# Kernel tuning notes

Measured on AMD Instinct MI355X. Metric: run time of the kernel, lower is better.

Reference implementation:

```python
import math
import jax, jax.numpy as jnp
import numpy as np

L, H, E, D = 12, 12, 768, 64   # stack_size, mh_size, embedding_dim, dim_w_matrices
B, S = 4, 512
EPS = 1e-5


def positional_enc(seq_len, model_dim):
    # faithful: power_ind = 10000 XOR int(2*i/dim)
    i = np.arange(model_dim)
    p = np.bitwise_xor(10000, (2 * i) // model_dim).astype(np.float32)
    pos = np.arange(seq_len, dtype=np.float32)[:, None]
    ang = pos / p[None, :]
    pe = np.where(i % 2 == 0, np.sin(ang), np.cos(ang)).astype(np.float32)
    return jnp.asarray(pe)


def layer_norm(x, g, b):
    mu = jnp.mean(x, axis=-1, keepdims=True)
    var = jnp.mean(jnp.square(x - mu), axis=-1, keepdims=True)
    return (x - mu) * jax.lax.rsqrt(var + EPS) * g + b


def encoder(x, wq, wo, g1, b1, fw, fb, g2, b2):
    # x: [B,S,E]; wq: [H,E,D]; wo: [E,H*D]; fw: [E,E] (torch Linear layout)
    bs = x.shape[0] * x.shape[1]
    nb = x.reshape(bs, E)                              # flatten batch (faithful)
    q = jnp.einsum('ne,hed->hnd', nb, wq)              # q == k == v (bug kept)
    scores = jax.nn.softmax(jnp.einsum('hnd,hmd->hnm', q, q) / math.sqrt(D), axis=-1)
    z = jnp.einsum('hnm,hmd->hnd', scores, q)          # [H,BS,D]
    zc = z.reshape(H * D, bs)                          # per-head view(D,-1) + cat
    mh = (wo @ zc).reshape(x.shape)                    # [B,S,E]
    l1 = layer_norm(x + mh, g1, b1)
    ffn = l1 @ fw.T + fb
    return layer_norm(l1 + ffn, g2, b2)


def setup_inputs() -> dict:
    key = jax.random.key(0)
    ks = jax.random.split(key, 8)

    def xavier(k, shape, fan_in, fan_out):
        lim = math.sqrt(6.0 / (fan_in + fan_out))
        return jax.random.uniform(k, shape, jnp.float32, -lim, lim)

    return {
        'tokens': jax.random.normal(ks[0], (B, S, E), jnp.float32),
        'wq':    xavier(ks[1], (L, H, E, D), E, D),
        'wo':    xavier(ks[2], (L, E, H * D), E, H * D),
        'ln1_g': jnp.ones((L, E), jnp.float32),
        'ln1_b': jnp.zeros((L, E), jnp.float32),
        'ffn_w': xavier(ks[3], (L, E, E), E, E),
        'ffn_b': jnp.zeros((L, E), jnp.float32),
        'ln2_g': jnp.ones((L, E), jnp.float32),
        'ln2_b': jnp.zeros((L, E), jnp.float32),
    }


def reference(tokens, wq, wo, ln1_g, ln1_b, ffn_w, ffn_b, ln2_g, ln2_b):
    pe = positional_enc(tokens.shape[1], tokens.shape[2])
    # faithful: layer 0 applied once on pe+tokens, then ALL layers (0 again) in loop
    x = encoder(pe + tokens, wq[0], wo[0], ln1_g[0], ln1_b[0],
                ffn_w[0], ffn_b[0], ln2_g[0], ln2_b[0])
    for l in range(L):
        x = encoder(x, wq[l], wo[l], ln1_g[l], ln1_b[l],
                    ffn_w[l], ffn_b[l], ln2_g[l], ln2_b[l])
    return x
```

## Files before the change

kernel.cpp:

```cpp
#include <hip/hip_runtime.h>
#include <hip/hip_bf16.h>


#define BS_TOK 2048
#define EMB 768
#define NH 12
#define HD 64
#define WQN (12 * NH * EMB * HD)

typedef __attribute__((ext_vector_type(8))) short bf16x8;
typedef __attribute__((ext_vector_type(4))) short bf16x4;
typedef __attribute__((ext_vector_type(4))) float f32x4;

__device__ __forceinline__ short f2bf(float f) {
  union { __hip_bfloat16 h; short s; } u;
  u.h = __float2bfloat16(f);
  return u.s;
}

#define MFMA16(a, b, c) __builtin_amdgcn_mfma_f32_16x16x32_bf16(a, b, c, 0, 0, 0)
#define SW64(r, k) ((r) * 64 + ((((k) >> 3) ^ ((r) & 7)) << 3) + ((k) & 7))
#define BAR() asm volatile("s_waitcnt lgkmcnt(0)\n\ts_barrier" ::: "memory")

__global__ __launch_bounds__(256) void cvt_weights_kernel(const float* __restrict__ wo,
                                                          const float* __restrict__ fw,
                                                          short* __restrict__ wob,
                                                          short* __restrict__ fwb) {
  const float* src = blockIdx.y ? fw : wo;
  short* dst = blockIdx.y ? fwb : wob;
  int i = (blockIdx.x * 256 + threadIdx.x) * 8;
  float4 a = *(const float4*)(src + i);
  float4 b = *(const float4*)(src + i + 4);
  bf16x8 t;
  t[0] = f2bf(a.x); t[1] = f2bf(a.y); t[2] = f2bf(a.z); t[3] = f2bf(a.w);
  t[4] = f2bf(b.x); t[5] = f2bf(b.y); t[6] = f2bf(b.z); t[7] = f2bf(b.w);
  *(bf16x8*)(dst + i) = t;
}

__global__ __launch_bounds__(256) void wq_trans_kernel(const float* __restrict__ wq,
                                                       short* __restrict__ wqT) {
  __shared__ short T[64 * 64];
  const int et = blockIdx.x;
  const int lh = blockIdx.y;
  const int tid = threadIdx.x;
  const float* src = wq + ((size_t)lh * EMB + et * 64) * HD;
  {
    int r = tid >> 2, c16 = (tid & 3) << 4;
    const float* p = src + r * HD + c16;
    float4 x0 = *(const float4*)(p + 0);
    float4 x1 = *(const float4*)(p + 4);
    float4 x2 = *(const float4*)(p + 8);
    float4 x3 = *(const float4*)(p + 12);
    bf16x8 a, b;
    a[0] = f2bf(x0.x); a[1] = f2bf(x0.y); a[2] = f2bf(x0.z); a[3] = f2bf(x0.w);
    a[4] = f2bf(x1.x); a[5] = f2bf(x1.y); a[6] = f2bf(x1.z); a[7] = f2bf(x1.w);
    b[0] = f2bf(x2.x); b[1] = f2bf(x2.y); b[2] = f2bf(x2.z); b[3] = f2bf(x2.w);
    b[4] = f2bf(x3.x); b[5] = f2bf(x3.y); b[6] = f2bf(x3.z); b[7] = f2bf(x3.w);
    int g = c16 >> 3;
    *(bf16x8*)&T[r * 64 + ((g ^ (r & 7)) << 3)] = a;
    *(bf16x8*)&T[r * 64 + (((g + 1) ^ (r & 7)) << 3)] = b;
  }
  __syncthreads();
  {
    int d = tid >> 2, e16 = (tid & 3) << 4;
    bf16x8 t0, t1;
#pragma unroll
    for (int j = 0; j < 8; ++j) t0[j] = T[SW64(e16 + j, d)];
#pragma unroll
    for (int j = 0; j < 8; ++j) t1[j] = T[SW64(e16 + 8 + j, d)];
    short* q = wqT + ((size_t)lh * HD + d) * EMB + et * 64 + e16;
    *(bf16x8*)(q) = t0;
    *(bf16x8*)(q + 8) = t1;
  }
}

__global__ __launch_bounds__(256) void pe_add_kernel(const float* __restrict__ tok,
                                                     float* __restrict__ X,
                                                     short* __restrict__ Xb) {
  int idx = blockIdx.x * 256 + threadIdx.x;
  int e = idx % EMB;
  int t = idx / EMB;
  int s = t & 511;
  float p = (e < 384) ? 10000.0f : 10001.0f;
  float ang = (float)s / p;
  float pe = (e & 1) ? cosf(ang) : sinf(ang);
  float v = tok[idx] + pe;
  X[idx] = v;
  Xb[idx] = f2bf(v);
}

__device__ __forceinline__ void load64(const short* __restrict__ src, int ld,
                                       int row0, int k0, bf16x8* r, int tid) {
  int rr = tid >> 2, kb = (tid & 3) << 4;
  const short* p = src + (size_t)(row0 + rr) * ld + k0 + kb;
  r[0] = *(const bf16x8*)(p);
  r[1] = *(const bf16x8*)(p + 8);
}
__device__ __forceinline__ void write64(short* dst, const bf16x8* r, int tid) {
  int rr = tid >> 2, g = (tid & 3) << 1;
  *(bf16x8*)&dst[rr * 64 + (((g + 0) ^ (rr & 7)) << 3)] = r[0];
  *(bf16x8*)&dst[rr * 64 + (((g + 1) ^ (rr & 7)) << 3)] = r[1];
}

__device__ __forceinline__ void load128(const short* __restrict__ src, int ld,
                                        int row0, int k0, bf16x8* r, int tid) {
  int rr = tid >> 1, kb = (tid & 1) << 5;
  const short* p = src + (size_t)(row0 + rr) * ld + k0 + kb;
  r[0] = *(const bf16x8*)(p);
  r[1] = *(const bf16x8*)(p + 8);
  r[2] = *(const bf16x8*)(p + 16);
  r[3] = *(const bf16x8*)(p + 24);
}
__device__ __forceinline__ void write128(short* dst, const bf16x8* r, int tid) {
  int rr = tid >> 1, g = (tid & 1) << 2;
#pragma unroll
  for (int i = 0; i < 4; ++i)
    *(bf16x8*)&dst[rr * 64 + (((g + i) ^ (rr & 7)) << 3)] = r[i];
}

__device__ __forceinline__ void load_zc(const short* __restrict__ Zcb,
                                        int k0, int col0, bf16x8 cr[2], int tid) {
  int kk = tid >> 2, nb = (tid & 3) << 4;
  const short* p = Zcb + (size_t)(k0 + kk) * BS_TOK + col0 + nb;
  cr[0] = *(const bf16x8*)(p);
  cr[1] = *(const bf16x8*)(p + 8);
}
__device__ __forceinline__ void write_zc(short* dst, const bf16x8 cr[2], int tid) {
  int kk = tid >> 2, nb = (tid & 3) << 4;
#pragma unroll
  for (int j = 0; j < 8; ++j) dst[SW64(nb + j, kk)] = cr[0][j];
#pragma unroll
  for (int j = 0; j < 8; ++j) dst[SW64(nb + 8 + j, kk)] = cr[1][j];
}

#define GEMM_TILE_COMPUTE(As, Bs, acc)                                              \
  {                                                                                 \
    _Pragma("unroll") for (int s = 0; s < 2; ++s) {                                 \
      int ra = (w << 4) + l15;                                                      \
      bf16x8 af = *(const bf16x8*)&As[ra * 64 + ((((s << 2) + quad) ^ (ra & 7)) << 3)]; \
      _Pragma("unroll") for (int nt = 0; nt < 4; ++nt) {                            \
        int rb = (nt << 4) + l15;                                                   \
        bf16x8 bf = *(const bf16x8*)&Bs[rb * 64 + ((((s << 2) + quad) ^ (rb & 7)) << 3)]; \
        acc[nt] = MFMA16(af, bf, acc[nt]);                                          \
      }                                                                             \
    }                                                                               \
  }

#define GEMM_TILE_COMPUTE2(As, Bs, acc)                                             \
  {                                                                                 \
    _Pragma("unroll") for (int s = 0; s < 2; ++s) {                                 \
      bf16x8 af[2];                                                                 \
      _Pragma("unroll") for (int u = 0; u < 2; ++u) {                               \
        int ra = (w << 5) + (u << 4) + l15;                                         \
        af[u] = *(const bf16x8*)&As[ra * 64 + ((((s << 2) + quad) ^ (ra & 7)) << 3)]; \
      }                                                                             \
      _Pragma("unroll") for (int nt = 0; nt < 4; ++nt) {                            \
        int rb = (nt << 4) + l15;                                                   \
        bf16x8 bf = *(const bf16x8*)&Bs[rb * 64 + ((((s << 2) + quad) ^ (rb & 7)) << 3)]; \
        acc[0][nt] = MFMA16(af[0], bf, acc[0][nt]);                                 \
        acc[1][nt] = MFMA16(af[1], bf, acc[1][nt]);                                 \
      }                                                                             \
    }                                                                               \
  }

__global__ __launch_bounds__(256) void gemm_q_kernel(const short* __restrict__ Xb,
                                                     const short* __restrict__ WqT,
                                                     short* __restrict__ Qo,
                                                     short* __restrict__ Qt) {
  __shared__ short As[2][64 * 64];
  __shared__ short Bs[2][64 * 64];
  const int m0 = blockIdx.x * 64;
  const int h = blockIdx.y;
  const int tid = threadIdx.x;
  const int w = tid >> 6, lane = tid & 63, l15 = lane & 15, quad = lane >> 4;
  const short* wqh = WqT + (size_t)h * (HD * EMB);
  f32x4 acc[4] = {};
  bf16x8 ar[2], br[2];
  load64(Xb, EMB, m0, 0, ar, tid);
  load64(wqh, EMB, 0, 0, br, tid);
  write64(As[0], ar, tid);
  write64(Bs[0], br, tid);
  load64(Xb, EMB, m0, 64, ar, tid);
  load64(wqh, EMB, 0, 64, br, tid);
  BAR();
  for (int k0 = 0; k0 < EMB; k0 += 64) {
    const int cur = (k0 >> 6) & 1;
    const short* Ac = As[cur];
    const short* Bc = Bs[cur];
    GEMM_TILE_COMPUTE(Ac, Bc, acc);
    if (k0 + 64 < EMB) {
      write64((short*)As[cur ^ 1], ar, tid);
      write64((short*)Bs[cur ^ 1], br, tid);
      if (k0 + 128 < EMB) {
        load64(Xb, EMB, m0, k0 + 128, ar, tid);
        load64(wqh, EMB, 0, k0 + 128, br, tid);
      }
    }
    BAR();
  }
  short* T = (short*)As[0];
#pragma unroll
  for (int nt = 0; nt < 4; ++nt)
#pragma unroll
    for (int r = 0; r < 4; ++r)
      T[SW64((w << 4) + (quad << 2) + r, (nt << 4) + l15)] = f2bf(acc[nt][r]);
  __syncthreads();
  {
    int r2 = tid >> 2, kb = (tid & 3) << 4;
    int g = kb >> 3;
    bf16x8 q0v = *(const bf16x8*)&T[r2 * 64 + ((g ^ (r2 & 7)) << 3)];
    bf16x8 q1v = *(const bf16x8*)&T[r2 * 64 + (((g + 1) ^ (r2 & 7)) << 3)];
    short* qo = Qo + (size_t)h * (BS_TOK * HD) + (size_t)(m0 + r2) * HD + kb;
    *(bf16x8*)(qo) = q0v;
    *(bf16x8*)(qo + 8) = q1v;
  }
  {
    int d = tid >> 2, tok0 = (tid & 3) << 4;
    bf16x8 t0, t1;
#pragma unroll
    for (int j = 0; j < 8; ++j) t0[j] = T[SW64(tok0 + j, d)];
#pragma unroll
    for (int j = 0; j < 8; ++j) t1[j] = T[SW64(tok0 + 8 + j, d)];
    short* qt = Qt + (size_t)h * (HD * BS_TOK) + (size_t)d * BS_TOK + m0 + tok0;
    *(bf16x8*)(qt) = t0;
    *(bf16x8*)(qt + 8) = t1;
  }
}

__global__ __launch_bounds__(256) void attn_mfma_kernel(const short* __restrict__ Q,
                                                        const short* __restrict__ Qt,
                                                        short* __restrict__ Zcb) {
  __shared__ short Ks[2][64 * 64];
  __shared__ short Vt[2][64 * 64];
  __shared__ short Pw[4][16 * 64];
  const int h = blockIdx.y;
  const int q0 = blockIdx.x * 64;
  const int tid = threadIdx.x;
  const int lane = tid & 63;
  const int wv = tid >> 6;
  const int l15 = lane & 15;
  const int quad = lane >> 4;
  const short* Qh = Q + (size_t)h * (BS_TOK * HD);
  const short* Qth = Qt + (size_t)h * (HD * BS_TOK);
  short* myP = Pw[wv];

  bf16x8 qf[2];
  {
    const short* qp = Qh + (size_t)(q0 + wv * 16 + l15) * HD + quad * 8;
    qf[0] = *(const bf16x8*)(qp);
    qf[1] = *(const bf16x8*)(qp + 32);
  }

  f32x4 o[4] = {};
  float lpl = 0.f;

  bf16x8 kreg[2], vreg[2];
#pragma unroll
  for (int i = 0; i < 2; ++i) {
    int c = i * 256 + tid;
    kreg[i] = *(const bf16x8*)(Qh + c * 8);
    vreg[i] = *(const bf16x8*)(Qth + (size_t)(c >> 3) * BS_TOK + (c & 7) * 8);
  }
#pragma unroll
  for (int i = 0; i < 2; ++i) {
    int c = i * 256 + tid, row = c >> 3, g = c & 7;
    *(bf16x8*)&Ks[0][row * 64 + ((g ^ (row & 7)) << 3)] = kreg[i];
    *(bf16x8*)&Vt[0][row * 64 + ((g ^ (row & 7)) << 3)] = vreg[i];
  }
#pragma unroll
  for (int i = 0; i < 2; ++i) {
    int c = i * 256 + tid;
    kreg[i] = *(const bf16x8*)(Qh + 4096 + c * 8);
    vreg[i] = *(const bf16x8*)(Qth + (size_t)(c >> 3) * BS_TOK + 64 + (c & 7) * 8);
  }
  BAR();

  for (int kt = 0; kt < 32; ++kt) {
    const short* K_ = Ks[kt & 1];
    const short* V_ = Vt[kt & 1];

    f32x4 s[4];
    __builtin_amdgcn_s_setprio(1);
#pragma unroll
    for (int ct = 0; ct < 4; ++ct) {
      f32x4 a = (f32x4){0.f, 0.f, 0.f, 0.f};
#pragma unroll
      for (int ks = 0; ks < 2; ++ks) {
        int row = ct * 16 + l15;
        int c = ks * 4 + quad;
        bf16x8 kf = *(const bf16x8*)(&K_[row * 64 + ((c ^ (row & 7)) << 3)]);
        a = MFMA16(kf, qf[ks], a);
      }
      s[ct] = a;
    }
    __builtin_amdgcn_s_setprio(0);

#pragma unroll
    for (int ct = 0; ct < 4; ++ct) {
      bf16x4 pv4;
#pragma unroll
      for (int r = 0; r < 4; ++r) {
        float p = exp2f(s[ct][r] * 0.18033688011112042f);
        lpl += p;
        pv4[r] = f2bf(p);
      }
      int g = 2 * ct + (quad >> 1);
      *(bf16x4*)&myP[l15 * 64 + ((g ^ (l15 & 7)) << 3) + ((quad & 1) << 2)] = pv4;
    }

    __builtin_amdgcn_s_setprio(1);
#pragma unroll
    for (int ks = 0; ks < 2; ++ks) {
      int c = ks * 4 + quad;
      bf16x8 pf = *(const bf16x8*)(&myP[l15 * 64 + ((c ^ (l15 & 7)) << 3)]);
#pragma unroll
      for (int dt = 0; dt < 4; ++dt) {
        int row = dt * 16 + l15;
        bf16x8 vf = *(const bf16x8*)(&V_[row * 64 + ((c ^ (row & 7)) << 3)]);
        o[dt] = MFMA16(pf, vf, o[dt]);
      }
    }
    __builtin_amdgcn_s_setprio(0);

    if (kt + 1 < 32) {
      short* Kn = (short*)Ks[(kt & 1) ^ 1];
      short* Vn = (short*)Vt[(kt & 1) ^ 1];
#pragma unroll
      for (int i = 0; i < 2; ++i) {
        int c = i * 256 + tid, row = c >> 3, g = c & 7;
        *(bf16x8*)&Kn[row * 64 + ((g ^ (row & 7)) << 3)] = kreg[i];
        *(bf16x8*)&Vn[row * 64 + ((g ^ (row & 7)) << 3)] = vreg[i];
      }
      if (kt + 2 < 32) {
        int gt = kt + 2;
#pragma unroll
        for (int i = 0; i < 2; ++i) {
          int c = i * 256 + tid;
          kreg[i] = *(const bf16x8*)(Qh + (size_t)gt * 4096 + c * 8);
          vreg[i] = *(const bf16x8*)(Qth + (size_t)(c >> 3) * BS_TOK + gt * 64 + (c & 7) * 8);
        }
      }
    }
    BAR();
  }

  lpl += __shfl_xor(lpl, 16, 64);
  lpl += __shfl_xor(lpl, 32, 64);

  float rl[4];
#pragma unroll
  for (int r = 0; r < 4; ++r)
    rl[r] = 1.0f / __shfl(lpl, quad * 4 + r, 64);

  short* T = (short*)Ks[0];
#pragma unroll
  for (int dt = 0; dt < 4; ++dt)
#pragma unroll
    for (int r = 0; r < 4; ++r)
      T[SW64(wv * 16 + quad * 4 + r, dt * 16 + l15)] = f2bf(o[dt][r] * rl[r]);
  __syncthreads();
  {
    short* zo = Zcb + (size_t)h * (BS_TOK * HD) + (size_t)q0 * HD;
    int r2 = tid >> 2, kb = (tid & 3) << 4;
    int g = kb >> 3;
    bf16x8 z0 = *(const bf16x8*)&T[r2 * 64 + ((g ^ (r2 & 7)) << 3)];
    bf16x8 z1 = *(const bf16x8*)&T[r2 * 64 + (((g + 1) ^ (r2 & 7)) << 3)];
    *(bf16x8*)(zo + r2 * 64 + kb) = z0;
    *(bf16x8*)(zo + r2 * 64 + kb + 8) = z1;
  }
}

__global__ __launch_bounds__(256) void gemm_out_kernel(const short* __restrict__ Wob,
                                                       const short* __restrict__ Zcb,
                                                       float* __restrict__ Pp) {
  __shared__ short As[2][128 * 64];
  __shared__ short Bs[2][64 * 64];
  const int n0 = blockIdx.x * 64;
  const int m0 = blockIdx.y * 128;
  const int kz = blockIdx.z * 384;
  const int tid = threadIdx.x;
  const int w = tid >> 6, lane = tid & 63, l15 = lane & 15, quad = lane >> 4;
  f32x4 acc[2][4] = {};
  bf16x8 ar[4], cr[2];
  load128(Wob, EMB, m0, kz, ar, tid);
  load_zc(Zcb, kz, n0, cr, tid);
  write128((short*)As[0], ar, tid);
  write_zc((short*)Bs[0], cr, tid);
  load128(Wob, EMB, m0, kz + 64, ar, tid);
  load_zc(Zcb, kz + 64, n0, cr, tid);
  BAR();
  for (int k0 = 0; k0 < 384; k0 += 64) {
    const int cur = (k0 >> 6) & 1;
    const short* Ac = As[cur];
    const short* Bc = Bs[cur];
    GEMM_TILE_COMPUTE2(Ac, Bc, acc);
    if (k0 + 64 < 384) {
      write128((short*)As[cur ^ 1], ar, tid);
      write_zc((short*)Bs[cur ^ 1], cr, tid);
      if (k0 + 128 < 384) {
        load128(Wob, EMB, m0, kz + k0 + 128, ar, tid);
        load_zc(Zcb, kz + k0 + 128, n0, cr, tid);
      }
    }
    BAR();
  }
  float* P = Pp + (size_t)blockIdx.z * (BS_TOK * EMB);
#pragma unroll
  for (int u = 0; u < 2; ++u)
#pragma unroll
    for (int nt = 0; nt < 4; ++nt)
#pragma unroll
      for (int r = 0; r < 4; ++r)
        P[(size_t)(m0 + (w << 5) + (u << 4) + (quad << 2) + r) * BS_TOK + n0 +
          (nt << 4) + l15] = acc[u][nt][r];
}

__global__ __launch_bounds__(256) void gemm_ffn_kernel(const short* __restrict__ L1b,
                                                       const short* __restrict__ Fwb,
                                                       const float* __restrict__ Fb,
                                                       float* __restrict__ Pp) {
  __shared__ short As[2][128 * 64];
  __shared__ short Bs[2][64 * 64];
  const int m0 = blockIdx.x * 128;
  const int n0 = blockIdx.y * 64;
  const int kz = blockIdx.z * 384;
  const int tid = threadIdx.x;
  const int w = tid >> 6, lane = tid & 63, l15 = lane & 15, quad = lane >> 4;
  f32x4 acc[2][4] = {};
  bf16x8 ar[4], br[2];
  load128(L1b, EMB, m0, kz, ar, tid);
  load64(Fwb, EMB, n0, kz, br, tid);
  write128((short*)As[0], ar, tid);
  write64((short*)Bs[0], br, tid);
  load128(L1b, EMB, m0, kz + 64, ar, tid);
  load64(Fwb, EMB, n0, kz + 64, br, tid);
  BAR();
  for (int k0 = 0; k0 < 384; k0 += 64) {
    const int cur = (k0 >> 6) & 1;
    const short* Ac = As[cur];
    const short* Bc = Bs[cur];
    GEMM_TILE_COMPUTE2(Ac, Bc, acc);
    if (k0 + 64 < 384) {
      write128((short*)As[cur ^ 1], ar, tid);
      write64((short*)Bs[cur ^ 1], br, tid);
      if (k0 + 128 < 384) {
        load128(L1b, EMB, m0, kz + k0 + 128, ar, tid);
        load64(Fwb, EMB, n0, kz + k0 + 128, br, tid);
      }
    }
    BAR();
  }
  float* P = Pp + (size_t)blockIdx.z * (BS_TOK * EMB);
  const bool addb = (blockIdx.z == 0);
#pragma unroll
  for (int nt = 0; nt < 4; ++nt) {
    float bias = addb ? Fb[n0 + (nt << 4) + l15] : 0.0f;
#pragma unroll
    for (int u = 0; u < 2; ++u)
#pragma unroll
      for (int r = 0; r < 4; ++r)
        P[(size_t)(m0 + (w << 5) + (u << 4) + (quad << 2) + r) * EMB + n0 +
          (nt << 4) + l15] = acc[u][nt][r] + bias;
  }
}

__global__ __launch_bounds__(256) void ln_kernel(const float* __restrict__ Xa,
                                                 const float* __restrict__ P,
                                                 const float* __restrict__ g,
                                                 const float* __restrict__ bb,
                                                 float* __restrict__ Out,
                                                 short* __restrict__ Outb) {
  const int NB = BS_TOK * EMB;
  const int wv = threadIdx.x >> 6, lane = threadIdx.x & 63;
  const int t = blockIdx.x * 4 + wv;
  const float* xa = Xa + (size_t)t * EMB;
  const float* p0 = P + (size_t)t * EMB;
  const float* p1 = p0 + NB;
  float4 v[3];
  float s = 0.f;
#pragma unroll
  for (int i = 0; i < 3; ++i) {
    int e = lane * 4 + i * 256;
    float4 a = *(const float4*)(xa + e);
    float4 b = *(const float4*)(p0 + e);
    float4 c = *(const float4*)(p1 + e);
    v[i].x = a.x + b.x + c.x;
    v[i].y = a.y + b.y + c.y;
    v[i].z = a.z + b.z + c.z;
    v[i].w = a.w + b.w + c.w;
    s += v[i].x + v[i].y + v[i].z + v[i].w;
  }
#pragma unroll
  for (int o = 32; o > 0; o >>= 1) s += __shfl_xor(s, o, 64);
  float mu = s * (1.0f / EMB);
  float q = 0.f;
#pragma unroll
  for (int i = 0; i < 3; ++i) {
    float dx = v[i].x - mu, dy = v[i].y - mu, dz = v[i].z - mu, dw = v[i].w - mu;
    q += dx * dx + dy * dy + dz * dz + dw * dw;
  }
#pragma unroll
  for (int o = 32; o > 0; o >>= 1) q += __shfl_xor(q, o, 64);
  float var = q * (1.0f / EMB);
  float r = rsqrtf(var + 1e-5f);
#pragma unroll
  for (int i = 0; i < 3; ++i) {
    int e = lane * 4 + i * 256;
    float4 gg = *(const float4*)(g + e);
    float4 bv = *(const float4*)(bb + e);
    float4 res;
    res.x = (v[i].x - mu) * r * gg.x + bv.x;
    res.y = (v[i].y - mu) * r * gg.y + bv.y;
    res.z = (v[i].z - mu) * r * gg.z + bv.z;
    res.w = (v[i].w - mu) * r * gg.w + bv.w;
    *(float4*)(Out + (size_t)t * EMB + e) = res;
    bf16x4 ob;
    ob[0] = f2bf(res.x);
    ob[1] = f2bf(res.y);
    ob[2] = f2bf(res.z);
    ob[3] = f2bf(res.w);
    *(bf16x4*)(Outb + (size_t)t * EMB + e) = ob;
  }
}

extern "C" void kernel_launch(void* const* d_in, const int* in_sizes, int n_in,
                              void* d_out, int out_size, void* d_ws, size_t ws_size,
                              hipStream_t stream) {
  const float* tok = (const float*)d_in[0];
  const float* wq = (const float*)d_in[1];
  const float* wo = (const float*)d_in[2];
  const float* g1 = (const float*)d_in[3];
  const float* b1 = (const float*)d_in[4];
  const float* fw = (const float*)d_in[5];
  const float* fb = (const float*)d_in[6];
  const float* g2 = (const float*)d_in[7];
  const float* b2 = (const float*)d_in[8];
  const int NB = BS_TOK * EMB;
  float* bufA = (float*)d_ws;
  float* bufB = bufA + NB;
  float* bufC = bufB + NB;
  float* bufD = bufC + NB;
  short* XbA = (short*)(bufD + NB);
  short* L1b = XbA + NB;
  short* Qbf = L1b + NB;
  short* Qtb = Qbf + NB;
  short* Zcb = Qtb + NB;
  short* wqTb = Zcb + NB;
  short* wob = wqTb + WQN;
  short* fwb = wob + WQN;

  cvt_weights_kernel<<<dim3(WQN / (256 * 8), 2), 256, 0, stream>>>(wo, fw, wob, fwb);
  wq_trans_kernel<<<dim3(12, 12 * NH), 256, 0, stream>>>(wq, wqTb);
  pe_add_kernel<<<NB / 256, 256, 0, stream>>>(tok, bufA, XbA);
  for (int it = 0; it < 13; ++it) {
    int l = (it == 0) ? 0 : it - 1;
    gemm_q_kernel<<<dim3(32, NH), 256, 0, stream>>>(
        XbA, wqTb + (size_t)l * (NH * HD * EMB), Qbf, Qtb);
    attn_mfma_kernel<<<dim3(32, NH), 256, 0, stream>>>(Qbf, Qtb, Zcb);
    gemm_out_kernel<<<dim3(32, 6, 2), 256, 0, stream>>>(
        wob + (size_t)l * (EMB * EMB), Zcb, bufB);
    ln_kernel<<<BS_TOK / 4, 256, 0, stream>>>(bufA, bufB, g1 + l * EMB, b1 + l * EMB,
                                              bufD, L1b);
    gemm_ffn_kernel<<<dim3(16, 12, 2), 256, 0, stream>>>(
        L1b, fwb + (size_t)l * (EMB * EMB), fb + l * EMB, bufB);
    float* ln2_dst = (it == 12) ? (float*)d_out : bufA;
    ln_kernel<<<BS_TOK / 4, 256, 0, stream>>>(bufD, bufB, g2 + l * EMB, b2 + l * EMB,
                                              ln2_dst, XbA);
  }
}
```

Baseline: 1.199 ms.

## Process two key tiles per barrier in attention with deeper LDS buffering

The attention loop now handles two 64-token K/V tiles per iteration, with four LDS buffers and two register prefetch sets. This halves the number of block barriers, and the LDS stores for the next pair are issued before compute instead of after it. Each wave gets two private P scratch buffers so the two tiles do not conflict. The cost is more LDS per block (about 80KB versus 40KB) and more prefetch registers, which may reduce occupancy.

Measured after the change: 1.179 ms. No clear change (-1.7%).

```diff
diff --git a/kernel.cpp b/kernel.cpp
--- a/kernel.cpp
+++ b/kernel.cpp
@@ -227,12 +227,60 @@
   }
 }
 
+__device__ __forceinline__ void attn_tile(const short* __restrict__ K_,
+                                          const short* __restrict__ V_,
+                                          short* __restrict__ P_,
+                                          const bf16x8 qf[2], f32x4 o[4],
+                                          float& lpl, int l15, int quad) {
+  f32x4 s[4];
+  __builtin_amdgcn_s_setprio(1);
+#pragma unroll
+  for (int ct = 0; ct < 4; ++ct) {
+    f32x4 a = (f32x4){0.f, 0.f, 0.f, 0.f};
+#pragma unroll
+    for (int ks = 0; ks < 2; ++ks) {
+      int row = ct * 16 + l15;
+      int c = ks * 4 + quad;
+      bf16x8 kf = *(const bf16x8*)(&K_[row * 64 + ((c ^ (row & 7)) << 3)]);
+      a = MFMA16(kf, qf[ks], a);
+    }
+    s[ct] = a;
+  }
+  __builtin_amdgcn_s_setprio(0);
+#pragma unroll
+  for (int ct = 0; ct < 4; ++ct) {
+    bf16x4 pv4;
+    float pp[4];
+#pragma unroll
+    for (int r = 0; r < 4; ++r) {
+      pp[r] = exp2f(s[ct][r] * 0.18033688011112042f);
+      pv4[r] = f2bf(pp[r]);
+    }
+    lpl += (pp[0] + pp[1]) + (pp[2] + pp[3]);
+    int g = 2 * ct + (quad >> 1);
+    *(bf16x4*)&P_[l15 * 64 + ((g ^ (l15 & 7)) << 3) + ((quad & 1) << 2)] = pv4;
+  }
+  __builtin_amdgcn_s_setprio(1);
+#pragma unroll
+  for (int ks = 0; ks < 2; ++ks) {
+    int c = ks * 4 + quad;
+    bf16x8 pf = *(const bf16x8*)(&P_[l15 * 64 + ((c ^ (l15 & 7)) << 3)]);
+#pragma unroll
+    for (int dt = 0; dt < 4; ++dt) {
+      int row = dt * 16 + l15;
+      bf16x8 vf = *(const bf16x8*)(&V_[row * 64 + ((c ^ (row & 7)) << 3)]);
+      o[dt] = MFMA16(pf, vf, o[dt]);
+    }
+  }
+  __builtin_amdgcn_s_setprio(0);
+}
+
 __global__ __launch_bounds__(256) void attn_mfma_kernel(const short* __restrict__ Q,
                                                         const short* __restrict__ Qt,
                                                         short* __restrict__ Zcb) {
-  __shared__ short Ks[2][64 * 64];
-  __shared__ short Vt[2][64 * 64];
-  __shared__ short Pw[4][16 * 64];
+  __shared__ short Ks[4][64 * 64];
+  __shared__ short Vt[4][64 * 64];
+  __shared__ short Pw[4][2][16 * 64];
   const int h = blockIdx.y;
   const int q0 = blockIdx.x * 64;
   const int tid = threadIdx.x;
@@ -242,7 +290,8 @@
   const int quad = lane >> 4;
   const short* Qh = Q + (size_t)h * (BS_TOK * HD);
   const short* Qth = Qt + (size_t)h * (HD * BS_TOK);
-  short* myP = Pw[wv];
+  short* myP0 = Pw[wv][0];
+  short* myP1 = Pw[wv][1];
 
   bf16x8 qf[2];
   {
@@ -254,93 +303,59 @@
   f32x4 o[4] = {};
   float lpl = 0.f;
 
-  bf16x8 kreg[2], vreg[2];
-#pragma unroll
-  for (int i = 0; i < 2; ++i) {
-    int c = i * 256 + tid;
-    kreg[i] = *(const bf16x8*)(Qh + c * 8);
-    vreg[i] = *(const bf16x8*)(Qth + (size_t)(c >> 3) * BS_TOK + (c & 7) * 8);
-  }
-#pragma unroll
-  for (int i = 0; i < 2; ++i) {
-    int c = i * 256 + tid, row = c >> 3, g = c & 7;
-    *(bf16x8*)&Ks[0][row * 64 + ((g ^ (row & 7)) << 3)] = kreg[i];
-    *(bf16x8*)&Vt[0][row * 64 + ((g ^ (row & 7)) << 3)] = vreg[i];
-  }
-#pragma unroll
-  for (int i = 0; i < 2; ++i) {
-    int c = i * 256 + tid;
-    kreg[i] = *(const bf16x8*)(Qh + 4096 + c * 8);
-    vreg[i] = *(const bf16x8*)(Qth + (size_t)(c >> 3) * BS_TOK + 64 + (c & 7) * 8);
-  }
+  bf16x8 kreg[2][2], vreg[2][2];
+#pragma unroll
+  for (int t = 0; t < 2; ++t)
+#pragma unroll
+    for (int i = 0; i < 2; ++i) {
+      int c = i * 256 + tid;
+      kreg[t][i] = *(const bf16x8*)(Qh + (size_t)t * 4096 + c * 8);
+      vreg[t][i] = *(const bf16x8*)(Qth + (size_t)(c >> 3) * BS_TOK + t * 64 + (c & 7) * 8);
+    }
+#pragma unroll
+  for (int t = 0; t < 2; ++t)
+#pragma unroll
+    for (int i = 0; i < 2; ++i) {
+      int c = i * 256 + tid, row = c >> 3, g = c & 7;
+      *(bf16x8*)&Ks[t][row * 64 + ((g ^ (row & 7)) << 3)] = kreg[t][i];
+      *(bf16x8*)&Vt[t][row * 64 + ((g ^ (row & 7)) << 3)] = vreg[t][i];
+    }
+#pragma unroll
+  for (int t = 0; t < 2; ++t)
+#pragma unroll
+    for (int i = 0; i < 2; ++i) {
+      int c = i * 256 + tid;
+      kreg[t][i] = *(const bf16x8*)(Qh + (size_t)(2 + t) * 4096 + c * 8);
+      vreg[t][i] = *(const bf16x8*)(Qth + (size_t)(c >> 3) * BS_TOK + (2 + t) * 64 + (c & 7) * 8);
+    }
   BAR();
 
-  for (int kt = 0; kt < 32; ++kt) {
-    const short* K_ = Ks[kt & 1];
-    const short* V_ = Vt[kt & 1];
-
-    f32x4 s[4];
-    __builtin_amdgcn_s_setprio(1);
-#pragma unroll
-    for (int ct = 0; ct < 4; ++ct) {
-      f32x4 a = (f32x4){0.f, 0.f, 0.f, 0.f};
-#pragma unroll
-      for (int ks = 0; ks < 2; ++ks) {
-        int row = ct * 16 + l15;
-        int c = ks * 4 + quad;
-        bf16x8 kf = *(const bf16x8*)(&K_[row * 64 + ((c ^ (row & 7)) << 3)]);
-        a = MFMA16(kf, qf[ks], a);
+  for (int p = 0; p < 16; ++p) {
+    const int base = (p & 1) * 2;
+    if (p + 1 < 16) {
+      const int nb = ((p + 1) & 1) * 2;
+#pragma unroll
+      for (int t = 0; t < 2; ++t)
+#pragma unroll
+        for (int i = 0; i < 2; ++i) {
+          int c = i * 256 + tid, row = c >> 3, g = c & 7;
+          *(bf16x8*)&Ks[nb + t][row * 64 + ((g ^ (row & 7)) << 3)] = kreg[t][i];
+          *(bf16x8*)&Vt[nb + t][row * 64 + ((g ^ (row & 7)) << 3)] = vreg[t][i];
+        }
+      if (p + 2 < 16) {
+        int gt0 = (p + 2) * 2;
+#pragma unroll
+        for (int t = 0; t < 2; ++t)
+#pragma unroll
+          for (int i = 0; i < 2; ++i) {
+            int c = i * 256 + tid;
+            kreg[t][i] = *(const bf16x8*)(Qh + (size_t)(gt0 + t) * 4096 + c * 8);
+            vreg[t][i] = *(const bf16x8*)(Qth + (size_t)(c >> 3) * BS_TOK + (gt0 + t) * 64 + (c & 7) * 8);
+          }
       }
-      s[ct] = a;
-    }
-    __builtin_amdgcn_s_setprio(0);
-
-#pragma unroll
-    for (int ct = 0; ct < 4; ++ct) {
-      bf16x4 pv4;
-#pragma unroll
-      for (int r = 0; r < 4; ++r) {
-        float p = exp2f(s[ct][r] * 0.18033688011112042f);
-        lpl += p;
-        pv4[r] = f2bf(p);
-      }
-      int g = 2 * ct + (quad >> 1);
-      *(bf16x4*)&myP[l15 * 64 + ((g ^ (l15 & 7)) << 3) + ((quad & 1) << 2)] = pv4;
-    }
-
-    __builtin_amdgcn_s_setprio(1);
-#pragma unroll
-    for (int ks = 0; ks < 2; ++ks) {
-      int c = ks * 4 + quad;
-      bf16x8 pf = *(const bf16x8*)(&myP[l15 * 64 + ((c ^ (l15 & 7)) << 3)]);
-#pragma unroll
-      for (int dt = 0; dt < 4; ++dt) {
-        int row = dt * 16 + l15;
-        bf16x8 vf = *(const bf16x8*)(&V_[row * 64 + ((c ^ (row & 7)) << 3)]);
-        o[dt] = MFMA16(pf, vf, o[dt]);
-      }
-    }
-    __builtin_amdgcn_s_setprio(0);
-
-    if (kt + 1 < 32) {
-      short* Kn = (short*)Ks[(kt & 1) ^ 1];
-      short* Vn = (short*)Vt[(kt & 1) ^ 1];
-#pragma unroll
-      for (int i = 0; i < 2; ++i) {
-        int c = i * 256 + tid, row = c >> 3, g = c & 7;
-        *(bf16x8*)&Kn[row * 64 + ((g ^ (row & 7)) << 3)] = kreg[i];
-        *(bf16x8*)&Vn[row * 64 + ((g ^ (row & 7)) << 3)] = vreg[i];
-      }
-      if (kt + 2 < 32) {
-        int gt = kt + 2;
-#pragma unroll
-        for (int i = 0; i < 2; ++i) {
-          int c = i * 256 + tid;
-          kreg[i] = *(const bf16x8*)(Qh + (size_t)gt * 4096 + c * 8);
-          vreg[i] = *(const bf16x8*)(Qth + (size_t)(c >> 3) * BS_TOK + gt * 64 + (c & 7) * 8);
-        }
-      }
-    }
+    }
+    attn_tile(Ks[base], Vt[base], myP0, qf, o, lpl, l15, quad);
+    attn_tile(Ks[base + 1], Vt[base + 1], myP1, qf, o, lpl, l15, quad);
     BAR();
   }
 
```
